# Optimization experiments

Measured on AMD Instinct MI355X. Metric: run time of the kernel, lower is better.

The kernel has to match this reference:

```python
import jax, jax.numpy as jnp
import numpy as np

N_NODES = 100000
N_EDGES = 1600000
D_IN = 64
D_OUT = 64


def setup_inputs() -> dict:
    key = jax.random.key(0)
    k1, k2, k3, k4 = jax.random.split(key, 4)
    x = jax.random.normal(k1, (N_NODES, D_IN), dtype=jnp.float32)
    edge_index = jax.random.randint(k2, (2, N_EDGES), 0, N_NODES, dtype=jnp.int64)
    W = jax.random.normal(k3, (D_OUT, D_IN), dtype=jnp.float32) * (1.0 / np.sqrt(D_IN))
    b = jax.random.normal(k4, (D_OUT,), dtype=jnp.float32) * 0.01
    return {"x": x, "edge_index": edge_index, "W": W, "b": b}


def reference(x, edge_index, W, b):
    num_nodes = x.shape[0]
    row, col = edge_index[0], edge_index[1]
    # degree of each node as a destination (scatter_add of ones over row)
    deg = jax.ops.segment_sum(jnp.ones(row.shape[0], dtype=x.dtype), row,
                              num_segments=num_nodes)
    # deg^-0.5 with inf (deg==0) replaced by 0
    deg_inv_sqrt = jnp.where(deg > 0, jax.lax.rsqrt(jnp.maximum(deg, 1.0)) * jnp.where(deg > 0, 1.0, 0.0), 0.0)
    deg_inv_sqrt = jnp.where(deg > 0, deg ** -0.5, 0.0)
    # gather source features, scale by source norm, scatter-add to destinations
    weighted = x[col] * deg_inv_sqrt[col][:, None]          # [E, D_IN]
    agg = jax.ops.segment_sum(weighted, row, num_segments=num_nodes)  # [N, D_IN]
    agg = agg * deg_inv_sqrt[:, None]
    # linear + relu (torch Linear: y = agg @ W.T + b)
    return jax.nn.relu(agg @ W.T + b)
```

## Files before the change

kernel.cpp:

```cpp
#include <hip/hip_runtime.h>

#define N_NODES 100000
#define N_EDGES 1600000
#define NE4 400000
#define D 64

#define CSHIFT 7
#define CNODES 128
#define NCB 782
#define CAPC 2560
#define COLBITS 17
#define COLMASK 0x1FFFF

#define EPB 8192
#define SBLKS 196
#define XBLKS 1563

#define CCUR_OFF   0
#define CPAIRS_OFF 3200
#define RS_OFF     8010880
#define DG_OFF     8410880
#define DINV_OFF   8810880
#define Y_OFF      9210880

typedef float fvec4 __attribute__((ext_vector_type(4)));
typedef __attribute__((ext_vector_type(8))) short bf16x8;
typedef __attribute__((ext_vector_type(4))) float f32x4;

__device__ __forceinline__ float bf2f(unsigned short u) {
    return __uint_as_float(((unsigned)u) << 16);
}
__device__ __forceinline__ unsigned f2bf(float f) {
    unsigned bits = __float_as_uint(f);
    return (bits + 0x7FFFu + ((bits >> 16) & 1u)) >> 16;
}

__global__ __launch_bounds__(256) void fat_kernel(
        const float* __restrict__ x, const float* __restrict__ W,
        const int* __restrict__ row, const int* __restrict__ col,
        int* __restrict__ ccur, int* __restrict__ cpairs,
        unsigned short* __restrict__ y) {
    __shared__ int lcnt[NCB];
    __shared__ int lbase[NCB];
    int t = threadIdx.x;
    if (blockIdx.x < SBLKS) {
        const int4* r4 = (const int4*)row;
        const int4* c4 = (const int4*)col;
        int base4 = blockIdx.x * (EPB / 4);
        for (int i = t; i < NCB; i += 256) lcnt[i] = 0;
        __syncthreads();
#pragma unroll
        for (int i = 0; i < EPB / 1024; ++i) {
            int i4 = base4 + i * 256 + t;
            if (i4 < NE4) {
                int4 rv = r4[i4];
                atomicAdd(&lcnt[rv.x >> CSHIFT], 1);
                atomicAdd(&lcnt[rv.y >> CSHIFT], 1);
                atomicAdd(&lcnt[rv.z >> CSHIFT], 1);
                atomicAdd(&lcnt[rv.w >> CSHIFT], 1);
            }
        }
        __syncthreads();
        for (int i = t; i < NCB; i += 256) {
            int cc = lcnt[i];
            lbase[i] = cc ? atomicAdd(&ccur[i], cc) : 0;
            lcnt[i] = 0;
        }
        __syncthreads();
#pragma unroll
        for (int i = 0; i < EPB / 1024; ++i) {
            int i4 = base4 + i * 256 + t;
            if (i4 < NE4) {
                int4 rv = r4[i4];
                int4 cv = c4[i4];
                int b0 = rv.x >> CSHIFT, b1 = rv.y >> CSHIFT;
                int b2 = rv.z >> CSHIFT, b3 = rv.w >> CSHIFT;
                int p0 = lbase[b0] + atomicAdd(&lcnt[b0], 1);
                int p1 = lbase[b1] + atomicAdd(&lcnt[b1], 1);
                int p2 = lbase[b2] + atomicAdd(&lcnt[b2], 1);
                int p3 = lbase[b3] + atomicAdd(&lcnt[b3], 1);
                if (p0 < CAPC) cpairs[(size_t)b0 * CAPC + p0] = ((rv.x & (CNODES - 1)) << COLBITS) | cv.x;
                if (p1 < CAPC) cpairs[(size_t)b1 * CAPC + p1] = ((rv.y & (CNODES - 1)) << COLBITS) | cv.y;
                if (p2 < CAPC) cpairs[(size_t)b2 * CAPC + p2] = ((rv.z & (CNODES - 1)) << COLBITS) | cv.z;
                if (p3 < CAPC) cpairs[(size_t)b3 * CAPC + p3] = ((rv.w & (CNODES - 1)) << COLBITS) | cv.w;
            }
        }
        return;
    }
    int wave = t >> 6, lane = t & 63;
    int n0w = (blockIdx.x - SBLKS) * 64 + wave * 16;
    if (n0w >= N_NODES) return;
    int lm = lane & 15;
    int g  = lane >> 4;
    bf16x8 ahi[2], alo[2];
    const float* xr = x + (size_t)(n0w + lm) * D + g * 8;
#pragma unroll
    for (int ks = 0; ks < 2; ++ks) {
        float4 fa = *(const float4*)(xr + ks * 32);
        float4 fb = *(const float4*)(xr + ks * 32 + 4);
        float f[8] = {fa.x, fa.y, fa.z, fa.w, fb.x, fb.y, fb.z, fb.w};
#pragma unroll
        for (int j = 0; j < 8; ++j) {
            unsigned hb = f2bf(f[j]);
            float r = f[j] - bf2f((unsigned short)hb);
            ahi[ks][j] = (short)hb;
            alo[ks][j] = (short)f2bf(r);
        }
    }
#pragma unroll
    for (int jt = 0; jt < 4; ++jt) {
        const float* wr = W + (size_t)(jt * 16 + lm) * D + g * 8;
        bf16x8 whi[2], wlo[2];
#pragma unroll
        for (int ks = 0; ks < 2; ++ks) {
            float4 fa = *(const float4*)(wr + ks * 32);
            float4 fb = *(const float4*)(wr + ks * 32 + 4);
            float f[8] = {fa.x, fa.y, fa.z, fa.w, fb.x, fb.y, fb.z, fb.w};
#pragma unroll
            for (int j = 0; j < 8; ++j) {
                unsigned hb = f2bf(f[j]);
                float r = f[j] - bf2f((unsigned short)hb);
                whi[ks][j] = (short)hb;
                wlo[ks][j] = (short)f2bf(r);
            }
        }
        f32x4 acc = {0.0f, 0.0f, 0.0f, 0.0f};
#pragma unroll
        for (int ks = 0; ks < 2; ++ks) {
            acc = __builtin_amdgcn_mfma_f32_16x16x32_bf16(ahi[ks], whi[ks], acc, 0, 0, 0);
            acc = __builtin_amdgcn_mfma_f32_16x16x32_bf16(alo[ks], whi[ks], acc, 0, 0, 0);
            acc = __builtin_amdgcn_mfma_f32_16x16x32_bf16(ahi[ks], wlo[ks], acc, 0, 0, 0);
        }
#pragma unroll
        for (int r = 0; r < 4; ++r) {
            int n = n0w + g * 4 + r;
            y[(size_t)n * D + jt * 16 + lm] = (unsigned short)f2bf(acc[r]);
        }
    }
}

__global__ __launch_bounds__(512) void scatB_kernel(const int* __restrict__ ccur,
                                                    int* __restrict__ cpairs,
                                                    int* __restrict__ rs,
                                                    int* __restrict__ dg,
                                                    float* __restrict__ dinv) {
    __shared__ int epk[CAPC];
    __shared__ int hist[CNODES];
    __shared__ int sc[CNODES];
    __shared__ int cur[CNODES];
    int t = threadIdx.x;
    int cb = blockIdx.x;
    int cnt = ccur[cb]; if (cnt > CAPC) cnt = CAPC;
    int base = cb * CAPC;
    if (t < CNODES) hist[t] = 0;
    __syncthreads();
    for (int i = t; i < cnt; i += 512) {
        int p = cpairs[base + i];
        epk[i] = p;
        atomicAdd(&hist[p >> COLBITS], 1);
    }
    __syncthreads();
    if (t < CNODES) sc[t] = hist[t];
    __syncthreads();
    for (int off = 1; off < CNODES; off <<= 1) {
        int v = (t < CNODES && t >= off) ? sc[t - off] : 0;
        __syncthreads();
        if (t < CNODES) sc[t] += v;
        __syncthreads();
    }
    if (t < CNODES) {
        int ex = sc[t] - hist[t];
        cur[t] = ex;
        int n = (cb << CSHIFT) + t;
        if (n < N_NODES) {
            rs[n] = base + ex;
            dg[n] = hist[t];
            dinv[n] = (hist[t] > 0) ? rsqrtf((float)hist[t]) : 0.0f;
        }
    }
    __syncthreads();
    for (int i = t; i < cnt; i += 512) {
        int p = epk[i];
        int pos = atomicAdd(&cur[p >> COLBITS], 1);
        cpairs[base + pos] = p & COLMASK;
    }
}

__global__ __launch_bounds__(256) void mega_kernel(
        const int* __restrict__ cols, const int* __restrict__ rs,
        const int* __restrict__ dg, const float* __restrict__ dinv,
        const unsigned short* __restrict__ y,
        const float* __restrict__ bias, float* __restrict__ out) {
    int t = threadIdx.x;
    int wave = t >> 6, lane = t & 63;
    int g = lane >> 3, q = lane & 7;
    int n = blockIdx.x * 32 + wave * 8 + g;
    int s = rs[n], d = dg[n];
    float bj[8];
    {
        float4 b0 = *(const float4*)(bias + q * 8);
        float4 b1 = *(const float4*)(bias + q * 8 + 4);
        bj[0] = b0.x; bj[1] = b0.y; bj[2] = b0.z; bj[3] = b0.w;
        bj[4] = b1.x; bj[5] = b1.y; bj[6] = b1.z; bj[7] = b1.w;
    }
    float a[8];
#pragma unroll
    for (int j = 0; j < 8; ++j) a[j] = 0.0f;
    int c8[8];
#pragma unroll
    for (int u = 0; u < 8; ++u) c8[u] = (u < d) ? cols[s + u] : 0;
    for (int k = 0; k < d; k += 8) {
        uint4 v[8];
        float dv8[8];
#pragma unroll
        for (int u = 0; u < 8; ++u) {
            if (k + u < d) {
                int c = c8[u];
                dv8[u] = dinv[c];
                v[u] = *(const uint4*)(y + (size_t)c * D + q * 8);
            }
        }
#pragma unroll
        for (int u = 0; u < 8; ++u) {
            int e2 = k + 8 + u;
            c8[u] = (e2 < d) ? cols[s + e2] : 0;
        }
#pragma unroll
        for (int u = 0; u < 8; ++u) {
            if (k + u < d) {
                float dvu = dv8[u];
                a[0] = fmaf(dvu, __uint_as_float(v[u].x << 16),         a[0]);
                a[1] = fmaf(dvu, __uint_as_float(v[u].x & 0xffff0000u), a[1]);
                a[2] = fmaf(dvu, __uint_as_float(v[u].y << 16),         a[2]);
                a[3] = fmaf(dvu, __uint_as_float(v[u].y & 0xffff0000u), a[3]);
                a[4] = fmaf(dvu, __uint_as_float(v[u].z << 16),         a[4]);
                a[5] = fmaf(dvu, __uint_as_float(v[u].z & 0xffff0000u), a[5]);
                a[6] = fmaf(dvu, __uint_as_float(v[u].w << 16),         a[6]);
                a[7] = fmaf(dvu, __uint_as_float(v[u].w & 0xffff0000u), a[7]);
            }
        }
    }
    float dvn = dinv[n];
    fvec4 r0, r1;
    r0.x = fmaxf(fmaf(dvn, a[0], bj[0]), 0.0f);
    r0.y = fmaxf(fmaf(dvn, a[1], bj[1]), 0.0f);
    r0.z = fmaxf(fmaf(dvn, a[2], bj[2]), 0.0f);
    r0.w = fmaxf(fmaf(dvn, a[3], bj[3]), 0.0f);
    r1.x = fmaxf(fmaf(dvn, a[4], bj[4]), 0.0f);
    r1.y = fmaxf(fmaf(dvn, a[5], bj[5]), 0.0f);
    r1.z = fmaxf(fmaf(dvn, a[6], bj[6]), 0.0f);
    r1.w = fmaxf(fmaf(dvn, a[7], bj[7]), 0.0f);
    __builtin_nontemporal_store(r0, (fvec4*)(out + (size_t)n * D + q * 8));
    __builtin_nontemporal_store(r1, (fvec4*)(out + (size_t)n * D + q * 8 + 4));
}

extern "C" void kernel_launch(void* const* d_in, const int* in_sizes, int n_in,
                              void* d_out, int out_size, void* d_ws, size_t ws_size,
                              hipStream_t stream) {
    const float* x    = (const float*)d_in[0];
    const int*   eidx = (const int*)d_in[1];
    const float* W    = (const float*)d_in[2];
    const float* b    = (const float*)d_in[3];
    float* out = (float*)d_out;
    char* ws = (char*)d_ws;

    const int* row = eidx;
    const int* col = eidx + N_EDGES;

    int* ccur   = (int*)(ws + CCUR_OFF);
    int* cpairs = (int*)(ws + CPAIRS_OFF);
    int* rs     = (int*)(ws + RS_OFF);
    int* dg     = (int*)(ws + DG_OFF);
    float* dinv = (float*)(ws + DINV_OFF);
    unsigned short* y = (unsigned short*)(ws + Y_OFF);

    hipMemsetAsync(ccur, 0, NCB * sizeof(int), stream);
    fat_kernel<<<SBLKS + XBLKS, 256, 0, stream>>>(x, W, row, col, ccur, cpairs, y);
    scatB_kernel<<<NCB, 512, 0, stream>>>(ccur, cpairs, rs, dg, dinv);
    mega_kernel<<<3125, 256, 0, stream>>>(cpairs, rs, dg, dinv, y, b, out);
}
```

Measured before the change: 152.1 us.

## Fuse CSR bucket sort with neighbor gather and compute degrees via global atomics

The per-bucket sort kernel and the gather/aggregate kernel become one kernel. Each 128-node bucket is sorted into shared memory and then aggregated directly, so the sorted column list and the row-start array are never written back to global memory. Node degrees are now counted with global atomics in the first kernel, and the inverse square roots are computed on the fly during the gather. This saves one launch and a round-trip of the edge list, but adds 1.6M global atomics and gives the gather only 782 blocks of 512 threads, which may lower occupancy and load balance compared with the previous 3125 blocks.

```diff
diff --git a/kernel.cpp b/kernel.cpp
--- a/kernel.cpp
+++ b/kernel.cpp
@@ -16,12 +16,10 @@
 #define SBLKS 196
 #define XBLKS 1563
 
-#define CCUR_OFF   0
-#define CPAIRS_OFF 3200
-#define RS_OFF     8010880
-#define DG_OFF     8410880
-#define DINV_OFF   8810880
-#define Y_OFF      9210880
+#define DG_OFF     0
+#define CCUR_OFF   401408
+#define CPAIRS_OFF 404608
+#define Y_OFF      8412288
 
 typedef float fvec4 __attribute__((ext_vector_type(4)));
 typedef __attribute__((ext_vector_type(8))) short bf16x8;
@@ -39,7 +37,7 @@
         const float* __restrict__ x, const float* __restrict__ W,
         const int* __restrict__ row, const int* __restrict__ col,
         int* __restrict__ ccur, int* __restrict__ cpairs,
-        unsigned short* __restrict__ y) {
+        int* __restrict__ dg, unsigned short* __restrict__ y) {
     __shared__ int lcnt[NCB];
     __shared__ int lbase[NCB];
     int t = threadIdx.x;
@@ -58,6 +56,10 @@
                 atomicAdd(&lcnt[rv.y >> CSHIFT], 1);
                 atomicAdd(&lcnt[rv.z >> CSHIFT], 1);
                 atomicAdd(&lcnt[rv.w >> CSHIFT], 1);
+                atomicAdd(&dg[rv.x], 1);
+                atomicAdd(&dg[rv.y], 1);
+                atomicAdd(&dg[rv.z], 1);
+                atomicAdd(&dg[rv.w], 1);
             }
         }
         __syncthreads();
@@ -139,19 +141,19 @@
     }
 }
 
-__global__ __launch_bounds__(512) void scatB_kernel(const int* __restrict__ ccur,
-                                                    int* __restrict__ cpairs,
-                                                    int* __restrict__ rs,
-                                                    int* __restrict__ dg,
-                                                    float* __restrict__ dinv) {
+__global__ __launch_bounds__(512) void gath_kernel(
+        const int* __restrict__ ccur, const int* __restrict__ cpairs,
+        const int* __restrict__ dg, const unsigned short* __restrict__ y,
+        const float* __restrict__ bias, float* __restrict__ out) {
     __shared__ int epk[CAPC];
+    __shared__ int scol[CAPC];
     __shared__ int hist[CNODES];
-    __shared__ int sc[CNODES];
+    __shared__ int lptr[CNODES + 1];
     __shared__ int cur[CNODES];
     int t = threadIdx.x;
     int cb = blockIdx.x;
+    int base = cb * CAPC;
     int cnt = ccur[cb]; if (cnt > CAPC) cnt = CAPC;
-    int base = cb * CAPC;
     if (t < CNODES) hist[t] = 0;
     __syncthreads();
     for (int i = t; i < cnt; i += 512) {
@@ -160,42 +162,29 @@
         atomicAdd(&hist[p >> COLBITS], 1);
     }
     __syncthreads();
-    if (t < CNODES) sc[t] = hist[t];
+    int hv = (t < CNODES) ? hist[t] : 0;
+    if (t < CNODES) cur[t] = hv;
     __syncthreads();
     for (int off = 1; off < CNODES; off <<= 1) {
-        int v = (t < CNODES && t >= off) ? sc[t - off] : 0;
-        __syncthreads();
-        if (t < CNODES) sc[t] += v;
+        int u = (t < CNODES && t >= off) ? cur[t - off] : 0;
+        __syncthreads();
+        if (t < CNODES) cur[t] += u;
         __syncthreads();
     }
     if (t < CNODES) {
-        int ex = sc[t] - hist[t];
-        cur[t] = ex;
-        int n = (cb << CSHIFT) + t;
-        if (n < N_NODES) {
-            rs[n] = base + ex;
-            dg[n] = hist[t];
-            dinv[n] = (hist[t] > 0) ? rsqrtf((float)hist[t]) : 0.0f;
-        }
-    }
+        lptr[t + 1] = cur[t];
+        cur[t] -= hv;
+    }
+    if (t == 0) lptr[0] = 0;
     __syncthreads();
     for (int i = t; i < cnt; i += 512) {
         int p = epk[i];
         int pos = atomicAdd(&cur[p >> COLBITS], 1);
-        cpairs[base + pos] = p & COLMASK;
-    }
-}
-
-__global__ __launch_bounds__(256) void mega_kernel(
-        const int* __restrict__ cols, const int* __restrict__ rs,
-        const int* __restrict__ dg, const float* __restrict__ dinv,
-        const unsigned short* __restrict__ y,
-        const float* __restrict__ bias, float* __restrict__ out) {
-    int t = threadIdx.x;
+        scol[pos] = p & COLMASK;
+    }
+    __syncthreads();
     int wave = t >> 6, lane = t & 63;
     int g = lane >> 3, q = lane & 7;
-    int n = blockIdx.x * 32 + wave * 8 + g;
-    int s = rs[n], d = dg[n];
     float bj[8];
     {
         float4 b0 = *(const float4*)(bias + q * 8);
@@ -203,55 +192,64 @@
         bj[0] = b0.x; bj[1] = b0.y; bj[2] = b0.z; bj[3] = b0.w;
         bj[4] = b1.x; bj[5] = b1.y; bj[6] = b1.z; bj[7] = b1.w;
     }
-    float a[8];
-#pragma unroll
-    for (int j = 0; j < 8; ++j) a[j] = 0.0f;
-    int c8[8];
-#pragma unroll
-    for (int u = 0; u < 8; ++u) c8[u] = (u < d) ? cols[s + u] : 0;
-    for (int k = 0; k < d; k += 8) {
-        uint4 v[8];
-        float dv8[8];
-#pragma unroll
-        for (int u = 0; u < 8; ++u) {
-            if (k + u < d) {
-                int c = c8[u];
-                dv8[u] = dinv[c];
-                v[u] = *(const uint4*)(y + (size_t)c * D + q * 8);
-            }
-        }
-#pragma unroll
-        for (int u = 0; u < 8; ++u) {
-            int e2 = k + 8 + u;
-            c8[u] = (e2 < d) ? cols[s + e2] : 0;
-        }
-#pragma unroll
-        for (int u = 0; u < 8; ++u) {
-            if (k + u < d) {
-                float dvu = dv8[u];
-                a[0] = fmaf(dvu, __uint_as_float(v[u].x << 16),         a[0]);
-                a[1] = fmaf(dvu, __uint_as_float(v[u].x & 0xffff0000u), a[1]);
-                a[2] = fmaf(dvu, __uint_as_float(v[u].y << 16),         a[2]);
-                a[3] = fmaf(dvu, __uint_as_float(v[u].y & 0xffff0000u), a[3]);
-                a[4] = fmaf(dvu, __uint_as_float(v[u].z << 16),         a[4]);
-                a[5] = fmaf(dvu, __uint_as_float(v[u].z & 0xffff0000u), a[5]);
-                a[6] = fmaf(dvu, __uint_as_float(v[u].w << 16),         a[6]);
-                a[7] = fmaf(dvu, __uint_as_float(v[u].w & 0xffff0000u), a[7]);
-            }
-        }
-    }
-    float dvn = dinv[n];
-    fvec4 r0, r1;
-    r0.x = fmaxf(fmaf(dvn, a[0], bj[0]), 0.0f);
-    r0.y = fmaxf(fmaf(dvn, a[1], bj[1]), 0.0f);
-    r0.z = fmaxf(fmaf(dvn, a[2], bj[2]), 0.0f);
-    r0.w = fmaxf(fmaf(dvn, a[3], bj[3]), 0.0f);
-    r1.x = fmaxf(fmaf(dvn, a[4], bj[4]), 0.0f);
-    r1.y = fmaxf(fmaf(dvn, a[5], bj[5]), 0.0f);
-    r1.z = fmaxf(fmaf(dvn, a[6], bj[6]), 0.0f);
-    r1.w = fmaxf(fmaf(dvn, a[7], bj[7]), 0.0f);
-    __builtin_nontemporal_store(r0, (fvec4*)(out + (size_t)n * D + q * 8));
-    __builtin_nontemporal_store(r1, (fvec4*)(out + (size_t)n * D + q * 8 + 4));
+#pragma unroll 1
+    for (int pass = 0; pass < 2; ++pass) {
+        int ln = pass * 64 + wave * 8 + g;
+        int n = (cb << CSHIFT) + ln;
+        int s = lptr[ln], d = lptr[ln + 1] - s;
+        float a[8];
+#pragma unroll
+        for (int j = 0; j < 8; ++j) a[j] = 0.0f;
+        int c8[8];
+#pragma unroll
+        for (int u = 0; u < 8; ++u) c8[u] = (u < d) ? scol[s + u] : 0;
+        for (int k = 0; k < d; k += 8) {
+            uint4 v[8];
+            float dv8[8];
+#pragma unroll
+            for (int u = 0; u < 8; ++u) {
+                if (k + u < d) {
+                    int c = c8[u];
+                    int dd = dg[c];
+                    dv8[u] = (dd > 0) ? rsqrtf((float)dd) : 0.0f;
+                    v[u] = *(const uint4*)(y + (size_t)c * D + q * 8);
+                }
+            }
+#pragma unroll
+            for (int u = 0; u < 8; ++u) {
+                int e2 = k + 8 + u;
+                c8[u] = (e2 < d) ? scol[s + e2] : 0;
+            }
+#pragma unroll
+            for (int u = 0; u < 8; ++u) {
+                if (k + u < d) {
+                    float dvu = dv8[u];
+                    a[0] = fmaf(dvu, __uint_as_float(v[u].x << 16),         a[0]);
+                    a[1] = fmaf(dvu, __uint_as_float(v[u].x & 0xffff0000u), a[1]);
+                    a[2] = fmaf(dvu, __uint_as_float(v[u].y << 16),         a[2]);
+                    a[3] = fmaf(dvu, __uint_as_float(v[u].y & 0xffff0000u), a[3]);
+                    a[4] = fmaf(dvu, __uint_as_float(v[u].z << 16),         a[4]);
+                    a[5] = fmaf(dvu, __uint_as_float(v[u].z & 0xffff0000u), a[5]);
+                    a[6] = fmaf(dvu, __uint_as_float(v[u].w << 16),         a[6]);
+                    a[7] = fmaf(dvu, __uint_as_float(v[u].w & 0xffff0000u), a[7]);
+                }
+            }
+        }
+        if (n < N_NODES) {
+            float dvn = (d > 0) ? rsqrtf((float)d) : 0.0f;
+            fvec4 r0, r1;
+            r0.x = fmaxf(fmaf(dvn, a[0], bj[0]), 0.0f);
+            r0.y = fmaxf(fmaf(dvn, a[1], bj[1]), 0.0f);
+            r0.z = fmaxf(fmaf(dvn, a[2], bj[2]), 0.0f);
+            r0.w = fmaxf(fmaf(dvn, a[3], bj[3]), 0.0f);
+            r1.x = fmaxf(fmaf(dvn, a[4], bj[4]), 0.0f);
+            r1.y = fmaxf(fmaf(dvn, a[5], bj[5]), 0.0f);
+            r1.z = fmaxf(fmaf(dvn, a[6], bj[6]), 0.0f);
+            r1.w = fmaxf(fmaf(dvn, a[7], bj[7]), 0.0f);
+            __builtin_nontemporal_store(r0, (fvec4*)(out + (size_t)n * D + q * 8));
+            __builtin_nontemporal_store(r1, (fvec4*)(out + (size_t)n * D + q * 8 + 4));
+        }
+    }
 }
 
 extern "C" void kernel_launch(void* const* d_in, const int* in_sizes, int n_in,
@@ -267,15 +265,12 @@
     const int* row = eidx;
     const int* col = eidx + N_EDGES;
 
+    int* dg     = (int*)(ws + DG_OFF);
     int* ccur   = (int*)(ws + CCUR_OFF);
     int* cpairs = (int*)(ws + CPAIRS_OFF);
-    int* rs     = (int*)(ws + RS_OFF);
-    int* dg     = (int*)(ws + DG_OFF);
-    float* dinv = (float*)(ws + DINV_OFF);
     unsigned short* y = (unsigned short*)(ws + Y_OFF);
 
-    hipMemsetAsync(ccur, 0, NCB * sizeof(int), stream);
-    fat_kernel<<<SBLKS + XBLKS, 256, 0, stream>>>(x, W, row, col, ccur, cpairs, y);
-    scatB_kernel<<<NCB, 512, 0, stream>>>(ccur, cpairs, rs, dg, dinv);
-    mega_kernel<<<3125, 256, 0, stream>>>(cpairs, rs, dg, dinv, y, b, out);
-}
+    hipMemsetAsync(dg, 0, CPAIRS_OFF, stream);
+    fat_kernel<<<SBLKS + XBLKS, 256, 0, stream>>>(x, W, row, col, ccur, cpairs, dg, y);
+    gath_kernel<<<NCB, 512, 0, stream>>>(ccur, cpairs, dg, y, b, out);
+}
```

New measurement: 209.9 us. 38.0% more time.

## Fuse per-bucket CSR scatter into aggregation kernel using shared-memory column lists

Applied to the files above, without the earlier changes.

Splits the old bucket-sort kernel into a light histogram/prefix kernel that emits row starts and dinv, and moves the local counting-sort scatter into the aggregation kernel, which now keeps each bucket's sorted column list in LDS. This removes the global write and re-read of the sorted cpairs array and the dg array. The aggregation grid drops from 3125 small blocks to 782 larger blocks, each handling 128 nodes in two passes. The sort-block edge count is also doubled (fewer sort blocks). Costs are fewer blocks for latency hiding, extra LDS per block, and a second read of cpairs.

```diff
diff --git a/kernel.cpp b/kernel.cpp
--- a/kernel.cpp
+++ b/kernel.cpp
@@ -12,16 +12,15 @@
 #define COLBITS 17
 #define COLMASK 0x1FFFF
 
-#define EPB 8192
-#define SBLKS 196
+#define EPB 16384
+#define SBLKS 98
 #define XBLKS 1563
 
 #define CCUR_OFF   0
 #define CPAIRS_OFF 3200
 #define RS_OFF     8010880
-#define DG_OFF     8410880
-#define DINV_OFF   8810880
-#define Y_OFF      9210880
+#define DINV_OFF   8412288
+#define Y_OFF      8813696
 
 typedef float fvec4 __attribute__((ext_vector_type(4)));
 typedef __attribute__((ext_vector_type(8))) short bf16x8;
@@ -139,63 +138,66 @@
     }
 }
 
-__global__ __launch_bounds__(512) void scatB_kernel(const int* __restrict__ ccur,
-                                                    int* __restrict__ cpairs,
-                                                    int* __restrict__ rs,
-                                                    int* __restrict__ dg,
-                                                    float* __restrict__ dinv) {
-    __shared__ int epk[CAPC];
+__global__ __launch_bounds__(256) void hist_kernel(
+        const int* __restrict__ ccur, const int* __restrict__ cpairs,
+        int* __restrict__ rs, float* __restrict__ dinv) {
     __shared__ int hist[CNODES];
     __shared__ int sc[CNODES];
-    __shared__ int cur[CNODES];
     int t = threadIdx.x;
     int cb = blockIdx.x;
+    int base = cb * CAPC;
     int cnt = ccur[cb]; if (cnt > CAPC) cnt = CAPC;
+    if (t < CNODES) hist[t] = 0;
+    __syncthreads();
+    for (int i = t; i < cnt; i += 256)
+        atomicAdd(&hist[cpairs[base + i] >> COLBITS], 1);
+    __syncthreads();
+    int hv = (t < CNODES) ? hist[t] : 0;
+    if (t < CNODES) sc[t] = hv;
+    __syncthreads();
+    for (int off = 1; off < CNODES; off <<= 1) {
+        int u = (t < CNODES && t >= off) ? sc[t - off] : 0;
+        __syncthreads();
+        if (t < CNODES) sc[t] += u;
+        __syncthreads();
+    }
+    if (t < CNODES) {
+        int n = (cb << CSHIFT) + t;
+        if (n < N_NODES) {
+            rs[n] = base + sc[t] - hv;
+            dinv[n] = (hv > 0) ? rsqrtf((float)hv) : 0.0f;
+        }
+    }
+}
+
+__global__ __launch_bounds__(512, 4) void megab_kernel(
+        const int* __restrict__ ccur, const int* __restrict__ cpairs,
+        const int* __restrict__ rs, const float* __restrict__ dinv,
+        const unsigned short* __restrict__ y,
+        const float* __restrict__ bias, float* __restrict__ out) {
+    __shared__ int scol[CAPC];
+    __shared__ int cur[CNODES];
+    __shared__ int sst[CNODES + 1];
+    int t = threadIdx.x;
+    int cb = blockIdx.x;
     int base = cb * CAPC;
-    if (t < CNODES) hist[t] = 0;
+    int cnt = ccur[cb]; if (cnt > CAPC) cnt = CAPC;
+    if (t < CNODES) {
+        int n = (cb << CSHIFT) + t;
+        int v = (n < N_NODES) ? rs[n] - base : cnt;
+        cur[t] = v;
+        sst[t] = v;
+    }
+    if (t == 0) sst[CNODES] = cnt;
     __syncthreads();
     for (int i = t; i < cnt; i += 512) {
         int p = cpairs[base + i];
-        epk[i] = p;
-        atomicAdd(&hist[p >> COLBITS], 1);
-    }
-    __syncthreads();
-    if (t < CNODES) sc[t] = hist[t];
-    __syncthreads();
-    for (int off = 1; off < CNODES; off <<= 1) {
-        int v = (t < CNODES && t >= off) ? sc[t - off] : 0;
-        __syncthreads();
-        if (t < CNODES) sc[t] += v;
-        __syncthreads();
-    }
-    if (t < CNODES) {
-        int ex = sc[t] - hist[t];
-        cur[t] = ex;
-        int n = (cb << CSHIFT) + t;
-        if (n < N_NODES) {
-            rs[n] = base + ex;
-            dg[n] = hist[t];
-            dinv[n] = (hist[t] > 0) ? rsqrtf((float)hist[t]) : 0.0f;
-        }
-    }
-    __syncthreads();
-    for (int i = t; i < cnt; i += 512) {
-        int p = epk[i];
         int pos = atomicAdd(&cur[p >> COLBITS], 1);
-        cpairs[base + pos] = p & COLMASK;
-    }
-}
-
-__global__ __launch_bounds__(256) void mega_kernel(
-        const int* __restrict__ cols, const int* __restrict__ rs,
-        const int* __restrict__ dg, const float* __restrict__ dinv,
-        const unsigned short* __restrict__ y,
-        const float* __restrict__ bias, float* __restrict__ out) {
-    int t = threadIdx.x;
+        scol[pos] = p & COLMASK;
+    }
+    __syncthreads();
     int wave = t >> 6, lane = t & 63;
     int g = lane >> 3, q = lane & 7;
-    int n = blockIdx.x * 32 + wave * 8 + g;
-    int s = rs[n], d = dg[n];
     float bj[8];
     {
         float4 b0 = *(const float4*)(bias + q * 8);
@@ -203,55 +205,63 @@
         bj[0] = b0.x; bj[1] = b0.y; bj[2] = b0.z; bj[3] = b0.w;
         bj[4] = b1.x; bj[5] = b1.y; bj[6] = b1.z; bj[7] = b1.w;
     }
-    float a[8];
-#pragma unroll
-    for (int j = 0; j < 8; ++j) a[j] = 0.0f;
-    int c8[8];
-#pragma unroll
-    for (int u = 0; u < 8; ++u) c8[u] = (u < d) ? cols[s + u] : 0;
-    for (int k = 0; k < d; k += 8) {
-        uint4 v[8];
-        float dv8[8];
-#pragma unroll
-        for (int u = 0; u < 8; ++u) {
-            if (k + u < d) {
-                int c = c8[u];
-                dv8[u] = dinv[c];
-                v[u] = *(const uint4*)(y + (size_t)c * D + q * 8);
-            }
-        }
-#pragma unroll
-        for (int u = 0; u < 8; ++u) {
-            int e2 = k + 8 + u;
-            c8[u] = (e2 < d) ? cols[s + e2] : 0;
-        }
-#pragma unroll
-        for (int u = 0; u < 8; ++u) {
-            if (k + u < d) {
-                float dvu = dv8[u];
-                a[0] = fmaf(dvu, __uint_as_float(v[u].x << 16),         a[0]);
-                a[1] = fmaf(dvu, __uint_as_float(v[u].x & 0xffff0000u), a[1]);
-                a[2] = fmaf(dvu, __uint_as_float(v[u].y << 16),         a[2]);
-                a[3] = fmaf(dvu, __uint_as_float(v[u].y & 0xffff0000u), a[3]);
-                a[4] = fmaf(dvu, __uint_as_float(v[u].z << 16),         a[4]);
-                a[5] = fmaf(dvu, __uint_as_float(v[u].z & 0xffff0000u), a[5]);
-                a[6] = fmaf(dvu, __uint_as_float(v[u].w << 16),         a[6]);
-                a[7] = fmaf(dvu, __uint_as_float(v[u].w & 0xffff0000u), a[7]);
-            }
-        }
-    }
-    float dvn = dinv[n];
-    fvec4 r0, r1;
-    r0.x = fmaxf(fmaf(dvn, a[0], bj[0]), 0.0f);
-    r0.y = fmaxf(fmaf(dvn, a[1], bj[1]), 0.0f);
-    r0.z = fmaxf(fmaf(dvn, a[2], bj[2]), 0.0f);
-    r0.w = fmaxf(fmaf(dvn, a[3], bj[3]), 0.0f);
-    r1.x = fmaxf(fmaf(dvn, a[4], bj[4]), 0.0f);
-    r1.y = fmaxf(fmaf(dvn, a[5], bj[5]), 0.0f);
-    r1.z = fmaxf(fmaf(dvn, a[6], bj[6]), 0.0f);
-    r1.w = fmaxf(fmaf(dvn, a[7], bj[7]), 0.0f);
-    __builtin_nontemporal_store(r0, (fvec4*)(out + (size_t)n * D + q * 8));
-    __builtin_nontemporal_store(r1, (fvec4*)(out + (size_t)n * D + q * 8 + 4));
+#pragma unroll 1
+    for (int pass = 0; pass < 2; ++pass) {
+        int ln = pass * 64 + wave * 8 + g;
+        int n = (cb << CSHIFT) + ln;
+        int s = sst[ln], d = sst[ln + 1] - s;
+        float a[8];
+#pragma unroll
+        for (int j = 0; j < 8; ++j) a[j] = 0.0f;
+        int c8[8];
+#pragma unroll
+        for (int u = 0; u < 8; ++u) c8[u] = (u < d) ? scol[s + u] : 0;
+        for (int k = 0; k < d; k += 8) {
+            uint4 v[8];
+            float dv8[8];
+#pragma unroll
+            for (int u = 0; u < 8; ++u) {
+                if (k + u < d) {
+                    int c = c8[u];
+                    dv8[u] = dinv[c];
+                    v[u] = *(const uint4*)(y + (size_t)c * D + q * 8);
+                }
+            }
+#pragma unroll
+            for (int u = 0; u < 8; ++u) {
+                int e2 = k + 8 + u;
+                c8[u] = (e2 < d) ? scol[s + e2] : 0;
+            }
+#pragma unroll
+            for (int u = 0; u < 8; ++u) {
+                if (k + u < d) {
+                    float dvu = dv8[u];
+                    a[0] = fmaf(dvu, __uint_as_float(v[u].x << 16),         a[0]);
+                    a[1] = fmaf(dvu, __uint_as_float(v[u].x & 0xffff0000u), a[1]);
+                    a[2] = fmaf(dvu, __uint_as_float(v[u].y << 16),         a[2]);
+                    a[3] = fmaf(dvu, __uint_as_float(v[u].y & 0xffff0000u), a[3]);
+                    a[4] = fmaf(dvu, __uint_as_float(v[u].z << 16),         a[4]);
+                    a[5] = fmaf(dvu, __uint_as_float(v[u].z & 0xffff0000u), a[5]);
+                    a[6] = fmaf(dvu, __uint_as_float(v[u].w << 16),         a[6]);
+                    a[7] = fmaf(dvu, __uint_as_float(v[u].w & 0xffff0000u), a[7]);
+                }
+            }
+        }
+        if (n < N_NODES) {
+            float dvn = dinv[n];
+            fvec4 r0, r1;
+            r0.x = fmaxf(fmaf(dvn, a[0], bj[0]), 0.0f);
+            r0.y = fmaxf(fmaf(dvn, a[1], bj[1]), 0.0f);
+            r0.z = fmaxf(fmaf(dvn, a[2], bj[2]), 0.0f);
+            r0.w = fmaxf(fmaf(dvn, a[3], bj[3]), 0.0f);
+            r1.x = fmaxf(fmaf(dvn, a[4], bj[4]), 0.0f);
+            r1.y = fmaxf(fmaf(dvn, a[5], bj[5]), 0.0f);
+            r1.z = fmaxf(fmaf(dvn, a[6], bj[6]), 0.0f);
+            r1.w = fmaxf(fmaf(dvn, a[7], bj[7]), 0.0f);
+            __builtin_nontemporal_store(r0, (fvec4*)(out + (size_t)n * D + q * 8));
+            __builtin_nontemporal_store(r1, (fvec4*)(out + (size_t)n * D + q * 8 + 4));
+        }
+    }
 }
 
 extern "C" void kernel_launch(void* const* d_in, const int* in_sizes, int n_in,
@@ -270,12 +280,11 @@
     int* ccur   = (int*)(ws + CCUR_OFF);
     int* cpairs = (int*)(ws + CPAIRS_OFF);
     int* rs     = (int*)(ws + RS_OFF);
-    int* dg     = (int*)(ws + DG_OFF);
     float* dinv = (float*)(ws + DINV_OFF);
     unsigned short* y = (unsigned short*)(ws + Y_OFF);
 
     hipMemsetAsync(ccur, 0, NCB * sizeof(int), stream);
     fat_kernel<<<SBLKS + XBLKS, 256, 0, stream>>>(x, W, row, col, ccur, cpairs, y);
-    scatB_kernel<<<NCB, 512, 0, stream>>>(ccur, cpairs, rs, dg, dinv);
-    mega_kernel<<<3125, 256, 0, stream>>>(cpairs, rs, dg, dinv, y, b, out);
-}
+    hist_kernel<<<NCB, 256, 0, stream>>>(ccur, cpairs, rs, dinv);
+    megab_kernel<<<NCB, 512, 0, stream>>>(ccur, cpairs, rs, dinv, y, b, out);
+}
```

After: 161.1 us. 1.06x slower.
